# Performance work log

Measured on AMD Instinct MI355X. Metric: run time of the kernel, lower is better.

The kernel has to match this reference:

```python
import jax, jax.numpy as jnp
import numpy as np

N_NODES = 50000
N_EDGES = 800000
N_GRAPHS = 256
FEAT = 128
HID = 64
HEADS = 4
OUT = 128
NEG_SLOPE = 0.2  # PyG GATConv default leaky_relu slope


def setup_inputs() -> dict:
    key = jax.random.key(0)
    ks = jax.random.split(key, 16)
    x = jax.random.normal(ks[0], (N_NODES, FEAT), dtype=jnp.float32)
    edge_index = jax.random.randint(ks[1], (2, N_EDGES), 0, N_NODES, dtype=jnp.int64)
    batch = jnp.sort(jax.random.randint(ks[2], (N_NODES,), 0, N_GRAPHS, dtype=jnp.int64))
    dims_in = [FEAT, HID * HEADS, HID * HEADS]
    params = {}
    for i, din in enumerate(dims_in):
        s = 1.0 / np.sqrt(din)
        params[f"W{i}"] = jax.random.normal(ks[3 + 4 * i], (din, HEADS * HID), dtype=jnp.float32) * s
        params[f"as{i}"] = jax.random.normal(ks[4 + 4 * i], (HEADS, HID), dtype=jnp.float32) * s
        params[f"ad{i}"] = jax.random.normal(ks[5 + 4 * i], (HEADS, HID), dtype=jnp.float32) * s
        params[f"b{i}"] = jnp.zeros((HEADS * HID,), dtype=jnp.float32)
    params["Wf"] = jax.random.normal(ks[15], (HID * HEADS, OUT), dtype=jnp.float32) / np.sqrt(HID * HEADS)
    params["bf"] = jnp.zeros((OUT,), dtype=jnp.float32)
    return {"x": x, "edge_index": edge_index, "batch": batch, **params}


def _gat_layer(x, src, dst, W, a_s, a_d, b):
    # x: [N, Din] -> h: [N, H, D]
    N = x.shape[0]
    h = (x @ W).reshape(N, HEADS, HID)
    alpha_src = jnp.einsum("nhd,hd->nh", h, a_s)  # [N, H]
    alpha_dst = jnp.einsum("nhd,hd->nh", h, a_d)
    e = jax.nn.leaky_relu(alpha_src[src] + alpha_dst[dst], NEG_SLOPE)  # [E, H]
    # segment softmax over edges sharing the same destination node
    m = jax.ops.segment_max(e, dst, num_segments=N)
    ex = jnp.exp(e - m[dst])
    s = jax.ops.segment_sum(ex, dst, num_segments=N)
    alpha = ex / s[dst]  # [E, H]
    msg = h[src] * alpha[:, :, None]  # [E, H, D]
    out = jax.ops.segment_sum(msg, dst, num_segments=N)  # [N, H, D]
    return out.reshape(N, HEADS * HID) + b


def reference(x, edge_index, batch, W0, as0, ad0, b0, W1, as1, ad1, b1,
              W2, as2, ad2, b2, Wf, bf):
    N = x.shape[0]
    loop = jnp.arange(N, dtype=edge_index.dtype)
    src = jnp.concatenate([edge_index[0], loop])  # PyG GATConv adds self-loops
    dst = jnp.concatenate([edge_index[1], loop])
    for W, a_s, a_d, b in ((W0, as0, ad0, b0), (W1, as1, ad1, b1), (W2, as2, ad2, b2)):
        x = jax.nn.elu(_gat_layer(x, src, dst, W, a_s, a_d, b))
    # global mean pool over graphs
    sums = jax.ops.segment_sum(x, batch, num_segments=N_GRAPHS)  # [G, HID*HEADS]
    cnt = jax.ops.segment_sum(jnp.ones((N,), x.dtype), batch, num_segments=N_GRAPHS)
    g = sums / jnp.maximum(cnt, 1.0)[:, None]
    y = g @ Wf + bf
    norm = jnp.linalg.norm(y, axis=-1, keepdims=True)
    return y / jnp.maximum(norm, 1e-12)
```

## Files before the change

### kernel.cpp

```cpp
#include <hip/hip_runtime.h>
#include <math.h>

#define NND 50000
#define NED 800000
#define ETOT 850000
#define NG 256
#define FEAT 128
#define CCH 256
#define OUTD 128
#define NEG 0.2f
#define NBLK 196
#define M2 50048
#define XBLK 6250

typedef __attribute__((ext_vector_type(8))) _Float16 half8;
typedef __attribute__((ext_vector_type(4))) _Float16 half4;
typedef __attribute__((ext_vector_type(4))) float floatx4;

#if __has_builtin(__builtin_amdgcn_global_load_lds)
#define GLOAD16(g, l) __builtin_amdgcn_global_load_lds( \
    (const __attribute__((address_space(1))) void*)(g), \
    (__attribute__((address_space(3))) void*)(l), 16, 0, 0)
#define HAVE_GLDS 1
#else
#define HAVE_GLDS 0
#endif


__global__ void count_kernel(const int* __restrict__ ei, int* __restrict__ deg) {
    int e = blockIdx.x * 256 + threadIdx.x;
    if (e >= ETOT) return;
    int dst = (e < NED) ? ei[NED + e] : (e - NED);
    atomicAdd(&deg[dst], 1);
}

__global__ __launch_bounds__(256) void scan_part_kernel(const int* __restrict__ deg,
                                                        int* __restrict__ bsum) {
    __shared__ int tile[256];
    int i = blockIdx.x * 256 + threadIdx.x;
    tile[threadIdx.x] = (i < NND) ? deg[i] : 0;
    __syncthreads();
    for (int s = 128; s > 0; s >>= 1) {
        if (threadIdx.x < s) tile[threadIdx.x] += tile[threadIdx.x + s];
        __syncthreads();
    }
    if (threadIdx.x == 0) bsum[blockIdx.x] = tile[0];
}

__global__ __launch_bounds__(256) void scan_bsum_kernel(int* __restrict__ bsum,
                                                        int* __restrict__ boff,
                                                        int* __restrict__ total) {
    __shared__ int tile[256];
    int t = threadIdx.x;
    int v = (t < NBLK) ? bsum[t] : 0;
    tile[t] = v;
    __syncthreads();
    for (int off = 1; off < 256; off <<= 1) {
        int u = (t >= off) ? tile[t - off] : 0;
        __syncthreads();
        tile[t] += u;
        __syncthreads();
    }
    if (t < NBLK) boff[t] = tile[t] - v;
    if (t == 255) *total = tile[255];
}

__global__ __launch_bounds__(256) void scan_write_kernel(const int* __restrict__ deg,
                                                         const int* __restrict__ boff,
                                                         const int* __restrict__ total,
                                                         int* __restrict__ rowptr,
                                                         int* __restrict__ cursor) {
    __shared__ int tile[256];
    int i = blockIdx.x * 256 + threadIdx.x;
    int t = threadIdx.x;
    int v = (i < NND) ? deg[i] : 0;
    tile[t] = v;
    __syncthreads();
    for (int off = 1; off < 256; off <<= 1) {
        int u = (t >= off) ? tile[t - off] : 0;
        __syncthreads();
        tile[t] += u;
        __syncthreads();
    }
    if (i < NND) {
        int r = boff[blockIdx.x] + tile[t] - v;
        rowptr[i] = r;
        cursor[i] = r;
    }
    if (i == 0) rowptr[NND] = *total;
}

__global__ void scatter_kernel(const int* __restrict__ ei, int* __restrict__ cursor,
                               int* __restrict__ csrsrc) {
    int e = blockIdx.x * 256 + threadIdx.x;
    if (e >= ETOT) return;
    int s, d;
    if (e < NED) { s = ei[e]; d = ei[NED + e]; } else { s = d = e - NED; }
    int pos = atomicAdd(&cursor[d], 1);
    csrsrc[pos] = s;
}


__global__ __launch_bounds__(256) void prep_kernel(const int* __restrict__ batch,
                                                   int* __restrict__ deg,
                                                   int* __restrict__ gstart,
                                                   const float4* __restrict__ x,
                                                   half4* __restrict__ xo,
                                                   const float* __restrict__ W0,
                                                   const float* __restrict__ W1,
                                                   const float* __restrict__ W2,
                                                   _Float16* __restrict__ wt0,
                                                   _Float16* __restrict__ wt1,
                                                   _Float16* __restrict__ wt2) {
    int b = blockIdx.x;
    if (b < 196) {
        int i = b * 256 + threadIdx.x;
        if (i < NND + 1) deg[i] = 0;
        return;
    }
    b -= 196;
    if (b < 196) {
        int i = b * 256 + threadIdx.x;
        if (i >= NND) return;
        int bb = batch[i];
        int bp = (i == 0) ? -1 : batch[i - 1];
        for (int g = bp + 1; g <= bb; ++g) gstart[g] = i;
        if (i == NND - 1)
            for (int g = bb + 1; g <= NG; ++g) gstart[g] = NND;
        return;
    }
    b -= 196;
    if (b < XBLK) {
        int i = b * 256 + threadIdx.x;
        if (i >= NND * FEAT / 4) return;
        float4 v = x[i];
        half4 o;
        o[0] = (_Float16)v.x; o[1] = (_Float16)v.y;
        o[2] = (_Float16)v.z; o[3] = (_Float16)v.w;
        xo[i] = o;
        return;
    }
    b -= XBLK;
    int j = b * 256 + threadIdx.x;
    if (j < 256 * 128) {
        int n = j >> 7, k = j & 127;
        wt0[j] = (_Float16)W0[k * 256 + n];
        return;
    }
    j -= 256 * 128;
    if (j < 256 * 256) {
        int n = j >> 8, k = j & 255;
        wt1[j] = (_Float16)W1[k * 256 + n];
        return;
    }
    j -= 256 * 256;
    if (j < 256 * 256) {
        int n = j >> 8, k = j & 255;
        wt2[j] = (_Float16)W2[k * 256 + n];
    }
}


#define BK 64

__global__ __launch_bounds__(256, 3) void gemm_mfma_kernel(
        const _Float16* __restrict__ A,
        const _Float16* __restrict__ Bt,
        const float* __restrict__ as_, const float* __restrict__ ad_,
        _Float16* __restrict__ Hm,
        float* __restrict__ asrc, float* __restrict__ adst, int K) {
    __shared__ _Float16 AsF[128 * 64];
    __shared__ _Float16 BsF[128 * 64];
    const int t = threadIdx.x;
    const int bn = blockIdx.x * 128;
    const int bm = blockIdx.y * 128;
    const int lane = t & 63, wv = t >> 6;
    const int wm = (wv >> 1) * 64, wn = (wv & 1) * 64;
    const int fr = lane & 15, q = lane >> 4;

    floatx4 acc[4][4] = {};

    const int lrow = t >> 3;
    const int c8 = t & 7;

    for (int k0 = 0; k0 < K; k0 += BK) {
        for (int p = 0; p < 4; p++) {
            int row = p * 32 + lrow;
            int g8 = c8 ^ (row & 7);
            const _Float16* ga = A + (size_t)(bm + row) * K + k0 + g8 * 8;
            const _Float16* gb = Bt + (size_t)(bn + row) * K + k0 + g8 * 8;
#if HAVE_GLDS
            GLOAD16(ga, &AsF[row * 64 + c8 * 8]);
            GLOAD16(gb, &BsF[row * 64 + c8 * 8]);
#else
            *(half8*)&AsF[row * 64 + c8 * 8] = *(const half8*)ga;
            *(half8*)&BsF[row * 64 + c8 * 8] = *(const half8*)gb;
#endif
        }
        __syncthreads();
        for (int kc = 0; kc < 2; kc++) {
            half8 af[4], bf[4];
            int kb = kc * 4 + q;
            int cs = (kb ^ (fr & 7)) * 8;
            for (int mi = 0; mi < 4; mi++)
                af[mi] = *(const half8*)&AsF[(wm + mi * 16 + fr) * 64 + cs];
            for (int ni = 0; ni < 4; ni++)
                bf[ni] = *(const half8*)&BsF[(wn + ni * 16 + fr) * 64 + cs];
            for (int mi = 0; mi < 4; mi++)
                for (int ni = 0; ni < 4; ni++)
                    acc[mi][ni] = __builtin_amdgcn_mfma_f32_16x16x32_f16(
                        af[mi], bf[ni], acc[mi][ni], 0, 0, 0);
        }
        __syncthreads();
    }

    for (int mi = 0; mi < 4; mi++) {
        int row0 = bm + wm + mi * 16 + q * 4;
        for (int ni = 0; ni < 4; ni++) {
            int col = bn + wn + ni * 16 + fr;
            for (int r = 0; r < 4; r++)
                Hm[(size_t)(row0 + r) * CCH + col] = (_Float16)acc[mi][ni][r];
        }
    }

    const int hd = (bn + wn) >> 6;
    float asf[4], adf[4];
    for (int ni = 0; ni < 4; ni++) {
        asf[ni] = as_[hd * 64 + ni * 16 + fr];
        adf[ni] = ad_[hd * 64 + ni * 16 + fr];
    }
    for (int mi = 0; mi < 4; mi++)
        for (int r = 0; r < 4; r++) {
            float ps = 0.f, pd = 0.f;
            for (int ni = 0; ni < 4; ni++) {
                float v = acc[mi][ni][r];
                ps += v * asf[ni];
                pd += v * adf[ni];
            }
            for (int m = 1; m < 16; m <<= 1) {
                ps += __shfl_xor(ps, m, 64);
                pd += __shfl_xor(pd, m, 64);
            }
            if (fr == 0) {
                int row = bm + wm + mi * 16 + q * 4 + r;
                asrc[row * 4 + hd] = ps;
                adst[row * 4 + hd] = pd;
            }
        }
}


__global__ __launch_bounds__(256) void agg_kernel(const _Float16* __restrict__ H16,
                                                  const float* __restrict__ asrc,
                                                  const float* __restrict__ adst,
                                                  const int* __restrict__ rowptr,
                                                  const int* __restrict__ csrsrc,
                                                  const float4* __restrict__ bias4,
                                                  half8* __restrict__ xo) {
    int wave = threadIdx.x >> 6, lane = threadIdx.x & 63;
    int n = blockIdx.x * 4 + wave;
    if (n >= NND) return;
    int rs = rowptr[n], re = rowptr[n + 1];
    int hd = lane >> 4;
    int sub = lane & 15;
    int l32 = lane & 31;
    int myh = l32 >> 3;
    int epar = lane >> 5;
    float adv = adst[n * 4 + hd];
    float acc[8] = {};
    float ssum = 0.f;
    const _Float16* hb = H16 + l32 * 8;

    int sl = rs + sub;
    bool ok = sl < re;
    int idx = ok ? csrsrc[sl] : 0;
    float aval = asrc[idx * 4 + hd];

    for (int e0 = rs; e0 < re; e0 += 16) {
        float ev = 0.f;
        if (ok) {
            float a = aval + adv;
            a = a > 0.f ? a : NEG * a;
            ev = __expf(a);
        }
        ssum += ev;
        int idxv = idx;
        int sl2 = e0 + 16 + sub;
        bool ok2 = sl2 < re;
        int idx2 = ok2 ? csrsrc[sl2] : 0;
        float aval2 = asrc[idx2 * 4 + hd];
        int cnt = re - e0; if (cnt > 16) cnt = 16;
        #pragma unroll
        for (int j2 = 0; j2 < 8; j2++) {
            if (j2 * 2 >= cnt) break;
            int j = j2 * 2 + epar;
            int s = __shfl(idxv, j, 64);
            float ww = __shfl(ev, myh * 16 + j, 64);
            half8 hv = *(const half8*)&hb[(size_t)s * CCH];
            #pragma unroll
            for (int k = 0; k < 8; k++) acc[k] += ww * (float)hv[k];
        }
        idx = idx2; aval = aval2; ok = ok2;
    }
    for (int off = 1; off < 16; off <<= 1) ssum += __shfl_xor(ssum, off, 64);
    float inv = 1.f / __shfl(ssum, myh * 16, 64);
    #pragma unroll
    for (int k = 0; k < 8; k++) acc[k] += __shfl_xor(acc[k], 32, 64);
    if (lane < 32) {
        float4 b0 = bias4[l32 * 2], b1 = bias4[l32 * 2 + 1];
        float o[8];
        o[0] = acc[0] * inv + b0.x; o[1] = acc[1] * inv + b0.y;
        o[2] = acc[2] * inv + b0.z; o[3] = acc[3] * inv + b0.w;
        o[4] = acc[4] * inv + b1.x; o[5] = acc[5] * inv + b1.y;
        o[6] = acc[6] * inv + b1.z; o[7] = acc[7] * inv + b1.w;
        half8 h;
        #pragma unroll
        for (int k = 0; k < 8; k++) {
            float v = o[k];
            v = v > 0.f ? v : expm1f(v);
            h[k] = (_Float16)v;
        }
        xo[(size_t)n * 32 + l32] = h;
    }
}


__global__ __launch_bounds__(256) void poolfinal_kernel(const _Float16* __restrict__ xa,
                                                        const int* __restrict__ gstart,
                                                        const float* __restrict__ Wf,
                                                        const float* __restrict__ bfv,
                                                        float* __restrict__ out) {
    int g = blockIdx.x, t = threadIdx.x;
    __shared__ float gm[256];
    __shared__ float red[128];
    int s = gstart[g], e = gstart[g + 1];
    float acc = 0.f;
    for (int i = s; i < e; i++)
        acc += (float)xa[(size_t)i * CCH + t];
    int cnt = e - s;
    gm[t] = acc / (float)(cnt > 0 ? cnt : 1);
    __syncthreads();
    float a = 0.f;
    if (t < OUTD) {
        a = bfv[t];
        for (int k = 0; k < CCH; k++) a += gm[k] * Wf[k * OUTD + t];
        red[t] = a * a;
    }
    __syncthreads();
    for (int sft = 64; sft > 0; sft >>= 1) {
        if (t < sft) red[t] += red[t + sft];
        __syncthreads();
    }
    if (t < OUTD) out[g * OUTD + t] = a / fmaxf(sqrtf(red[0]), 1e-12f);
}


extern "C" void kernel_launch(void* const* d_in, const int* in_sizes, int n_in,
                              void* d_out, int out_size, void* d_ws, size_t ws_size,
                              hipStream_t stream) {
    const float* x     = (const float*)d_in[0];
    const int*   ei    = (const int*)d_in[1];
    const int*   batch = (const int*)d_in[2];
    const float* W[3]  = {(const float*)d_in[3], (const float*)d_in[7],  (const float*)d_in[11]};
    const float* As[3] = {(const float*)d_in[4], (const float*)d_in[8],  (const float*)d_in[12]};
    const float* Ad[3] = {(const float*)d_in[5], (const float*)d_in[9],  (const float*)d_in[13]};
    const float* Bb[3] = {(const float*)d_in[6], (const float*)d_in[10], (const float*)d_in[14]};
    const float* Wf    = (const float*)d_in[15];
    const float* bf    = (const float*)d_in[16];
    float* out = (float*)d_out;

    _Float16* H16   = (_Float16*)d_ws;
    _Float16* act16 = H16 + (size_t)M2 * CCH;
    _Float16* wt0   = act16 + (size_t)M2 * CCH;
    _Float16* wt1   = wt0 + 256 * 128;
    _Float16* wt2   = wt1 + 256 * 256;
    float* asrc  = (float*)(wt2 + 256 * 256);
    float* adst  = asrc + (size_t)M2 * 4;
    int* deg     = (int*)(adst + (size_t)M2 * 4);
    int* rowptr  = deg + (NND + 1);
    int* cursor  = rowptr + (NND + 1);
    int* csrsrc  = cursor + (NND + 1);
    int* gstart  = csrsrc + ETOT;
    int* bsum    = gstart + (NG + 1);
    int* boff    = bsum + NBLK;
    int* total   = boff + NBLK;

    _Float16* wt[3] = {wt0, wt1, wt2};

    prep_kernel<<<196 + 196 + XBLK + 640, 256, 0, stream>>>(
        batch, deg, gstart, (const float4*)x, (half4*)act16,
        W[0], W[1], W[2], wt0, wt1, wt2);
    count_kernel<<<(ETOT + 255) / 256, 256, 0, stream>>>(ei, deg);
    scan_part_kernel<<<NBLK, 256, 0, stream>>>(deg, bsum);
    scan_bsum_kernel<<<1, 256, 0, stream>>>(bsum, boff, total);
    scan_write_kernel<<<NBLK, 256, 0, stream>>>(deg, boff, total, rowptr, cursor);
    scatter_kernel<<<(ETOT + 255) / 256, 256, 0, stream>>>(ei, cursor, csrsrc);

    int K = FEAT;
    for (int l = 0; l < 3; l++) {
        dim3 g(2, M2 / 128);
        gemm_mfma_kernel<<<g, 256, 0, stream>>>(act16, wt[l], As[l], Ad[l], H16, asrc, adst, K);
        agg_kernel<<<(NND + 3) / 4, 256, 0, stream>>>(H16, asrc, adst, rowptr, csrsrc,
                                                      (const float4*)Bb[l], (half8*)act16);
        K = CCH;
    }

    poolfinal_kernel<<<NG, 256, 0, stream>>>(act16, gstart, Wf, bf, out);
}
```

Before: 513.1 us.

## Fuse CSR construction kernels into one cooperative kernel with grid syncs

Replaces the five CSR-building launches (count, three scan stages, scatter) and the degree-zeroing part of prep with a single cooperative kernel of 196 blocks that uses grid.sync between phases. The goal is to remove kernel launch gaps and tail effects across the short stages. The trade-off is that count and scatter now run on only 196 blocks with grid-stride loops, which lowers parallelism for the atomic-heavy edge passes, and grid.sync itself has a cost.

```diff
diff --git a/kernel.cpp b/kernel.cpp
--- a/kernel.cpp
+++ b/kernel.cpp
@@ -1,5 +1,8 @@
 #include <hip/hip_runtime.h>
+#include <hip/hip_cooperative_groups.h>
 #include <math.h>
+
+namespace cg = cooperative_groups;
 
 #define NND 50000
 #define NED 800000
@@ -27,82 +30,89 @@
 #endif
 
 
-__global__ void count_kernel(const int* __restrict__ ei, int* __restrict__ deg) {
-    int e = blockIdx.x * 256 + threadIdx.x;
-    if (e >= ETOT) return;
-    int dst = (e < NED) ? ei[NED + e] : (e - NED);
-    atomicAdd(&deg[dst], 1);
-}
-
-__global__ __launch_bounds__(256) void scan_part_kernel(const int* __restrict__ deg,
-                                                        int* __restrict__ bsum) {
+__global__ __launch_bounds__(256) void csr_coop_kernel(const int* __restrict__ ei,
+                                                       int* __restrict__ deg,
+                                                       int* __restrict__ rowptr,
+                                                       int* __restrict__ cursor,
+                                                       int* __restrict__ csrsrc,
+                                                       int* __restrict__ bsum,
+                                                       int* __restrict__ boff,
+                                                       int* __restrict__ total) {
+    cg::grid_group grid = cg::this_grid();
     __shared__ int tile[256];
-    int i = blockIdx.x * 256 + threadIdx.x;
-    tile[threadIdx.x] = (i < NND) ? deg[i] : 0;
-    __syncthreads();
-    for (int s = 128; s > 0; s >>= 1) {
-        if (threadIdx.x < s) tile[threadIdx.x] += tile[threadIdx.x + s];
-        __syncthreads();
-    }
-    if (threadIdx.x == 0) bsum[blockIdx.x] = tile[0];
-}
-
-__global__ __launch_bounds__(256) void scan_bsum_kernel(int* __restrict__ bsum,
-                                                        int* __restrict__ boff,
-                                                        int* __restrict__ total) {
-    __shared__ int tile[256];
-    int t = threadIdx.x;
-    int v = (t < NBLK) ? bsum[t] : 0;
-    tile[t] = v;
-    __syncthreads();
-    for (int off = 1; off < 256; off <<= 1) {
-        int u = (t >= off) ? tile[t - off] : 0;
-        __syncthreads();
-        tile[t] += u;
-        __syncthreads();
-    }
-    if (t < NBLK) boff[t] = tile[t] - v;
-    if (t == 255) *total = tile[255];
-}
-
-__global__ __launch_bounds__(256) void scan_write_kernel(const int* __restrict__ deg,
-                                                         const int* __restrict__ boff,
-                                                         const int* __restrict__ total,
-                                                         int* __restrict__ rowptr,
-                                                         int* __restrict__ cursor) {
-    __shared__ int tile[256];
-    int i = blockIdx.x * 256 + threadIdx.x;
-    int t = threadIdx.x;
-    int v = (i < NND) ? deg[i] : 0;
-    tile[t] = v;
-    __syncthreads();
-    for (int off = 1; off < 256; off <<= 1) {
-        int u = (t >= off) ? tile[t - off] : 0;
-        __syncthreads();
-        tile[t] += u;
-        __syncthreads();
-    }
-    if (i < NND) {
-        int r = boff[blockIdx.x] + tile[t] - v;
-        rowptr[i] = r;
-        cursor[i] = r;
-    }
-    if (i == 0) rowptr[NND] = *total;
-}
-
-__global__ void scatter_kernel(const int* __restrict__ ei, int* __restrict__ cursor,
-                               int* __restrict__ csrsrc) {
-    int e = blockIdx.x * 256 + threadIdx.x;
-    if (e >= ETOT) return;
-    int s, d;
-    if (e < NED) { s = ei[e]; d = ei[NED + e]; } else { s = d = e - NED; }
-    int pos = atomicAdd(&cursor[d], 1);
-    csrsrc[pos] = s;
+    const int t = threadIdx.x;
+    const int b = blockIdx.x;
+    const int gid = b * 256 + t;
+    const int gsz = gridDim.x * 256;
+
+    for (int i = gid; i < NND + 1; i += gsz) deg[i] = 0;
+    grid.sync();
+
+    for (int e = gid; e < ETOT; e += gsz) {
+        int dst = (e < NED) ? ei[NED + e] : (e - NED);
+        atomicAdd(&deg[dst], 1);
+    }
+    grid.sync();
+
+    {
+        int i = b * 256 + t;
+        tile[t] = (i < NND) ? deg[i] : 0;
+        __syncthreads();
+        for (int s = 128; s > 0; s >>= 1) {
+            if (t < s) tile[t] += tile[t + s];
+            __syncthreads();
+        }
+        if (t == 0) bsum[b] = tile[0];
+    }
+    grid.sync();
+
+    if (b == 0) {
+        int v = (t < NBLK) ? bsum[t] : 0;
+        __syncthreads();
+        tile[t] = v;
+        __syncthreads();
+        for (int off = 1; off < 256; off <<= 1) {
+            int u = (t >= off) ? tile[t - off] : 0;
+            __syncthreads();
+            tile[t] += u;
+            __syncthreads();
+        }
+        if (t < NBLK) boff[t] = tile[t] - v;
+        if (t == 255) *total = tile[255];
+    }
+    grid.sync();
+
+    {
+        int i = b * 256 + t;
+        int v = (i < NND) ? deg[i] : 0;
+        __syncthreads();
+        tile[t] = v;
+        __syncthreads();
+        for (int off = 1; off < 256; off <<= 1) {
+            int u = (t >= off) ? tile[t - off] : 0;
+            __syncthreads();
+            tile[t] += u;
+            __syncthreads();
+        }
+        if (i < NND) {
+            int r = boff[b] + tile[t] - v;
+            rowptr[i] = r;
+            cursor[i] = r;
+        }
+        if (i == 0) rowptr[NND] = *total;
+    }
+    grid.sync();
+
+    for (int e = gid; e < ETOT; e += gsz) {
+        int s, d;
+        if (e < NED) { s = ei[e]; d = ei[NED + e]; } else { s = d = e - NED; }
+        int pos = atomicAdd(&cursor[d], 1);
+        csrsrc[pos] = s;
+    }
 }
 
 
 __global__ __launch_bounds__(256) void prep_kernel(const int* __restrict__ batch,
-                                                   int* __restrict__ deg,
                                                    int* __restrict__ gstart,
                                                    const float4* __restrict__ x,
                                                    half4* __restrict__ xo,
@@ -113,12 +123,6 @@
                                                    _Float16* __restrict__ wt1,
                                                    _Float16* __restrict__ wt2) {
     int b = blockIdx.x;
-    if (b < 196) {
-        int i = b * 256 + threadIdx.x;
-        if (i < NND + 1) deg[i] = 0;
-        return;
-    }
-    b -= 196;
     if (b < 196) {
         int i = b * 256 + threadIdx.x;
         if (i >= NND) return;
@@ -387,14 +391,16 @@
 
     _Float16* wt[3] = {wt0, wt1, wt2};
 
-    prep_kernel<<<196 + 196 + XBLK + 640, 256, 0, stream>>>(
-        batch, deg, gstart, (const float4*)x, (half4*)act16,
+    prep_kernel<<<196 + XBLK + 640, 256, 0, stream>>>(
+        batch, gstart, (const float4*)x, (half4*)act16,
         W[0], W[1], W[2], wt0, wt1, wt2);
-    count_kernel<<<(ETOT + 255) / 256, 256, 0, stream>>>(ei, deg);
-    scan_part_kernel<<<NBLK, 256, 0, stream>>>(deg, bsum);
-    scan_bsum_kernel<<<1, 256, 0, stream>>>(bsum, boff, total);
-    scan_write_kernel<<<NBLK, 256, 0, stream>>>(deg, boff, total, rowptr, cursor);
-    scatter_kernel<<<(ETOT + 255) / 256, 256, 0, stream>>>(ei, cursor, csrsrc);
+
+    {
+        void* args[] = {(void*)&ei, (void*)&deg, (void*)&rowptr, (void*)&cursor,
+                        (void*)&csrsrc, (void*)&bsum, (void*)&boff, (void*)&total};
+        hipLaunchCooperativeKernel((void*)csr_coop_kernel, dim3(NBLK), dim3(256),
+                                   args, 0, stream);
+    }
 
     int K = FEAT;
     for (int l = 0; l < 3; l++) {
```

Result: slower. 633.8 us (+23.5%).
